# Performance work log

Hardware: AMD Instinct MI355X
Metric: run time of the kernel (lower is better)

## Reference

```python
import jax, jax.numpy as jnp
from jax import lax
import numpy as np

D_MODEL, D_STATE, D_CONV, EXPAND = 1024, 16, 4, 2
D_INNER = EXPAND * D_MODEL          # 2048
DT_RANK = D_MODEL // 16             # 64
B_SZ, L_SEQ = 2, 2048


def setup_inputs() -> dict:
    key = jax.random.key(0)
    ks = jax.random.split(key, 8)
    x = jax.random.normal(ks[0], (B_SZ, L_SEQ, D_MODEL), jnp.float32)
    inp = {
        "x": x,
        "ln_g": jnp.ones((D_MODEL,), jnp.float32),
        "ln_b": jnp.zeros((D_MODEL,), jnp.float32),
        # fan-in scaled weights for numerical sanity
        "W_in": jax.random.normal(ks[1], (2 * D_INNER, D_MODEL), jnp.float32) / np.sqrt(D_MODEL),
        "conv_w": jax.random.normal(ks[2], (D_INNER, D_CONV), jnp.float32) / np.sqrt(D_CONV),
        "conv_b": jnp.zeros((D_INNER,), jnp.float32),
        "W_xp": jax.random.normal(ks[3], (DT_RANK + 2 * D_STATE, D_INNER), jnp.float32) / np.sqrt(D_INNER),
        "W_dt": jax.random.normal(ks[4], (D_INNER, DT_RANK), jnp.float32) / np.sqrt(DT_RANK),
        "b_dt": jax.random.normal(ks[5], (D_INNER,), jnp.float32) * 0.1 - 4.0,  # softplus(dt) small, like mamba init
        # S4D-real init: A = -exp(A_log), A_log = log(1..d_state)
        "A_log": jnp.broadcast_to(jnp.log(jnp.arange(1, D_STATE + 1, dtype=jnp.float32)), (D_INNER, D_STATE)).copy(),
        "D": jnp.ones((D_INNER,), jnp.float32),
        "W_out": jax.random.normal(ks[6], (D_MODEL, D_INNER), jnp.float32) / np.sqrt(D_INNER),
    }
    return inp


def _selective_scan(u, dt, A, Bm, Cm, Dvec):
    # u, dt: (B, L, d_inner); Bm, Cm: (B, L, d_state); A: (d_inner, d_state)
    def step(h, inputs):
        u_t, dt_t, B_t, C_t = inputs                      # (B,di),(B,di),(B,n),(B,n)
        dA = jnp.exp(dt_t[:, :, None] * A[None])          # (B,di,n), in (0,1) since A<0
        dBu = (dt_t * u_t)[:, :, None] * B_t[:, None, :]  # (B,di,n)
        h = dA * h + dBu
        y = jnp.einsum('bdn,bn->bd', h, C_t)
        return h, y
    xs = (u.transpose(1, 0, 2), dt.transpose(1, 0, 2),
          Bm.transpose(1, 0, 2), Cm.transpose(1, 0, 2))
    h0 = jnp.zeros((u.shape[0], u.shape[2], A.shape[1]), u.dtype)
    _, ys = lax.scan(step, h0, xs)
    return ys.transpose(1, 0, 2) + u * Dvec               # (B, L, d_inner)


def reference(x, ln_g, ln_b, W_in, conv_w, conv_b, W_xp, W_dt, b_dt, A_log, D, W_out):
    d_inner, d_conv = conv_w.shape
    dt_rank = W_dt.shape[1]
    d_state = A_log.shape[1]
    # pre-LayerNorm
    mu = jnp.mean(x, axis=-1, keepdims=True)
    var = jnp.mean(jnp.square(x - mu), axis=-1, keepdims=True)
    xn = (x - mu) * lax.rsqrt(var + 1e-5) * ln_g + ln_b
    # input projection -> (B, L, 2*d_inner)
    xz = jnp.einsum('bld,ed->ble', xn, W_in)
    u, z = jnp.split(xz, 2, axis=-1)
    # causal depthwise conv over time
    u_c = lax.conv_general_dilated(
        u.transpose(0, 2, 1),                 # (B, d_inner, L)
        conv_w[:, None, :],                   # (d_inner, 1, d_conv)
        window_strides=(1,), padding=[(d_conv - 1, 0)],
        feature_group_count=d_inner)
    u_c = jax.nn.silu((u_c + conv_b[None, :, None]).transpose(0, 2, 1))  # (B, L, d_inner)
    # data-dependent dt, B, C
    x_dbl = jnp.einsum('bld,ed->ble', u_c, W_xp)
    dt, Bm, Cm = jnp.split(x_dbl, [dt_rank, dt_rank + d_state], axis=-1)
    dt = jax.nn.softplus(jnp.einsum('blr,dr->bld', dt, W_dt) + b_dt)
    A = -jnp.exp(A_log)
    y = _selective_scan(u_c, dt, A, Bm, Cm, D)
    y = y * jax.nn.silu(z)
    out = jnp.einsum('ble,de->bld', y, W_out)
    return x + out
```

## Files before the change

### kernel.cpp

```cpp
#include <hip/hip_runtime.h>

typedef __bf16 bf16x8 __attribute__((ext_vector_type(8)));
typedef float  f32x4  __attribute__((ext_vector_type(4)));

#define LOG2E 1.44269504088896f

__device__ __forceinline__ float bfl(unsigned short s) {
    return __uint_as_float(((unsigned int)s) << 16);
}
__device__ __forceinline__ unsigned short f2bf(float f) {
    unsigned int x = __float_as_uint(f);
    x += 0x7fffu + ((x >> 16) & 1u);
    return (unsigned short)(x >> 16);
}
__device__ __forceinline__ float fexp2(float x) { return __builtin_amdgcn_exp2f(x); }
__device__ __forceinline__ float fexp(float x)  { return __builtin_amdgcn_exp2f(x * LOG2E); }
__device__ __forceinline__ float frcp(float x)  { return __builtin_amdgcn_rcpf(x); }
__device__ __forceinline__ float silu_f(float x) {
    return x * frcp(1.f + fexp2(-x * LOG2E));
}
__device__ __forceinline__ void gl_lds(const unsigned short* g, unsigned short* l) {
    __builtin_amdgcn_global_load_lds(
        (__attribute__((address_space(1))) const void*)g,
        (__attribute__((address_space(3))) void*)l, 16, 0, 0);
}

#define BSZ   2
#define LSEQ  2048
#define DMODEL 1024
#define DI    2048
#define DS    16
#define NCH   64
#define CL    32

#define WI_N   4194304
#define WXP_N  196608
#define WDT_N  131072
#define WOUT_N 2097152
#define WSEG1  (WI_N)
#define WSEG2  (WI_N + WXP_N)
#define WSEG3  (WI_N + WXP_N + WDT_N)
#define WTOT   (WI_N + WXP_N + WDT_N + WOUT_N)

__global__ __launch_bounds__(256) void cvt_weights(
    const float* __restrict__ w0, const float* __restrict__ w1,
    const float* __restrict__ w2, const float* __restrict__ w3,
    unsigned short* __restrict__ dst)
{
    const size_t e0 = ((size_t)blockIdx.x * 256 + threadIdx.x) * 8;
    if (e0 >= WTOT) return;
    const float* src;
    size_t off;
    if      (e0 < WSEG1) { src = w0; off = e0; }
    else if (e0 < WSEG2) { src = w1; off = e0 - WSEG1; }
    else if (e0 < WSEG3) { src = w2; off = e0 - WSEG2; }
    else                 { src = w3; off = e0 - WSEG3; }
    float4 a = *(const float4*)(src + off);
    float4 b = *(const float4*)(src + off + 4);
    ushort4 lo, hi;
    lo.x = f2bf(a.x); lo.y = f2bf(a.y); lo.z = f2bf(a.z); lo.w = f2bf(a.w);
    hi.x = f2bf(b.x); hi.y = f2bf(b.y); hi.z = f2bf(b.z); hi.w = f2bf(b.w);
    *(ushort4*)(dst + e0) = lo;
    *(ushort4*)(dst + e0 + 4) = hi;
}

__global__ __launch_bounds__(256) void ln_kernel(
    const float* __restrict__ x,
    const float* __restrict__ g,
    const float* __restrict__ b,
    unsigned short* __restrict__ xn)
{
    const int row = blockIdx.x;
    const int tid = threadIdx.x;
    const int lane = tid & 63, wv = tid >> 6;
    const float* xp = x + (size_t)row * DMODEL;

    float4 v = ((const float4*)xp)[tid];
    float s = v.x + v.y + v.z + v.w;
    float q = v.x*v.x + v.y*v.y + v.z*v.z + v.w*v.w;
    #pragma unroll
    for (int o = 32; o > 0; o >>= 1) {
        s += __shfl_down(s, o);
        q += __shfl_down(q, o);
    }
    __shared__ float ss[4], sq[4];
    if (lane == 0) { ss[wv] = s; sq[wv] = q; }
    __syncthreads();
    s = ss[0] + ss[1] + ss[2] + ss[3];
    q = sq[0] + sq[1] + sq[2] + sq[3];
    const float mu  = s * (1.f / DMODEL);
    const float var = q * (1.f / DMODEL) - mu * mu;
    const float rs  = rsqrtf(var + 1e-5f);

    float4 gv = ((const float4*)g)[tid];
    float4 bv = ((const float4*)b)[tid];
    ushort4 o;
    o.x = f2bf((v.x - mu) * rs * gv.x + bv.x);
    o.y = f2bf((v.y - mu) * rs * gv.y + bv.y);
    o.z = f2bf((v.z - mu) * rs * gv.z + bv.z);
    o.w = f2bf((v.w - mu) * rs * gv.w + bv.w);
    ((ushort4*)(xn + (size_t)row * DMODEL))[tid] = o;
}

template<int EPI, int LOGM>
__global__ __launch_bounds__(512, 2) void gemm_pipe(
    const unsigned short* __restrict__ A,
    const unsigned short* __restrict__ Bw,
    void* __restrict__ Cout,
    const void* __restrict__ aux0,
    int K, int ldc)
{
    __shared__ unsigned short As[2][256 * 64];
    __shared__ unsigned short Bs[2][128 * 64];
    const int tid  = threadIdx.x;
    const int lane = tid & 63;
    const int wid  = tid >> 6;
    const int wm   = (wid >> 2) * 128;
    const int wn   = (wid & 3) * 32;

    const int nwg = gridDim.x;
    const int id  = blockIdx.x;
    const int swz = (id & 7) * (nwg >> 3) + (id >> 3);
    const int bx  = swz & ((1 << LOGM) - 1);
    const int by  = swz >> LOGM;
    const size_t am0 = (size_t)bx * 256;
    const size_t bn0 = (size_t)by * 128;

    const int srow  = lane >> 3;
    const int sslot = (lane & 7) ^ srow;
    const unsigned short* gA = A  + (am0 + wid * 32 + srow) * (size_t)K + sslot * 8;
    const unsigned short* gB = Bw + (bn0 + wid * 16 + srow) * (size_t)K + sslot * 8;
    unsigned short* lA0 = &As[0][(wid * 32) * 64];
    unsigned short* lB0 = &Bs[0][(wid * 16) * 64];
    unsigned short* lA1 = &As[1][(wid * 32) * 64];
    unsigned short* lB1 = &Bs[1][(wid * 16) * 64];

    const int NT = K >> 6;
    #pragma unroll
    for (int j = 0; j < 4; ++j) gl_lds(gA + (size_t)(8 * j) * K,       lA0 + j * 512);
    #pragma unroll
    for (int j = 0; j < 2; ++j) gl_lds(gB + (size_t)(8 * j) * K,       lB0 + j * 512);
    #pragma unroll
    for (int j = 0; j < 4; ++j) gl_lds(gA + (size_t)(8 * j) * K + 64,  lA1 + j * 512);
    #pragma unroll
    for (int j = 0; j < 2; ++j) gl_lds(gB + (size_t)(8 * j) * K + 64,  lB1 + j * 512);

    f32x4 acc[8][2];
    f32x4 z4 = {0.f, 0.f, 0.f, 0.f};
    #pragma unroll
    for (int i = 0; i < 8; ++i) { acc[i][0] = z4; acc[i][1] = z4; }

    const int lr  = lane & 15;
    const int lq  = lane >> 4;
    const int key = lr & 7;

    for (int t = 0; t < NT; ++t) {
        const int cur = t & 1;
        if (t < NT - 1) asm volatile("s_waitcnt vmcnt(6)" ::: "memory");
        else            asm volatile("s_waitcnt vmcnt(0)" ::: "memory");
        __builtin_amdgcn_s_barrier();
        __builtin_amdgcn_sched_barrier(0);

        bf16x8 af[8][2], bfv[2][2];
        #pragma unroll
        for (int fm = 0; fm < 8; ++fm)
            #pragma unroll
            for (int ks = 0; ks < 2; ++ks)
                af[fm][ks] = *(const bf16x8*)
                    &As[cur][(wm + fm * 16 + lr) * 64 + ((ks * 4 + lq) ^ key) * 8];
        #pragma unroll
        for (int fn = 0; fn < 2; ++fn)
            #pragma unroll
            for (int ks = 0; ks < 2; ++ks)
                bfv[fn][ks] = *(const bf16x8*)
                    &Bs[cur][(wn + fn * 16 + lr) * 64 + ((ks * 4 + lq) ^ key) * 8];
        asm volatile("s_waitcnt lgkmcnt(0)" ::: "memory");
        __builtin_amdgcn_sched_barrier(0);
        __builtin_amdgcn_s_barrier();

        if (t + 2 < NT) {
            const size_t ko = (size_t)(t + 2) * 64;
            unsigned short* dA = (cur ? lA1 : lA0);
            unsigned short* dB = (cur ? lB1 : lB0);
            #pragma unroll
            for (int j = 0; j < 4; ++j) gl_lds(gA + (size_t)(8 * j) * K + ko, dA + j * 512);
            #pragma unroll
            for (int j = 0; j < 2; ++j) gl_lds(gB + (size_t)(8 * j) * K + ko, dB + j * 512);
        }

        __builtin_amdgcn_s_setprio(1);
        #pragma unroll
        for (int fm = 0; fm < 8; ++fm)
            #pragma unroll
            for (int fn = 0; fn < 2; ++fn) {
                acc[fm][fn] = __builtin_amdgcn_mfma_f32_16x16x32_bf16(
                    af[fm][0], bfv[fn][0], acc[fm][fn], 0, 0, 0);
                acc[fm][fn] = __builtin_amdgcn_mfma_f32_16x16x32_bf16(
                    af[fm][1], bfv[fn][1], acc[fm][fn], 0, 0, 0);
            }
        __builtin_amdgcn_s_setprio(0);
    }

    const int er = lq * 4;
    const int ec = lr;
    #pragma unroll
    for (int fm = 0; fm < 8; ++fm) {
        #pragma unroll
        for (int fn = 0; fn < 2; ++fn) {
            const size_t col = bn0 + wn + fn * 16 + ec;
            #pragma unroll
            for (int r = 0; r < 4; ++r) {
                const size_t row = am0 + wm + fm * 16 + er + r;
                float v = acc[fm][fn][r];
                if constexpr (EPI == 0) {
                    ((unsigned short*)Cout)[row * ldc + col] = f2bf(v);
                } else {
                    float t2 = v + ((const float*)aux0)[row * ldc + col];
                    ((float*)Cout)[row * ldc + col] = t2;
                }
            }
        }
    }
}

template<int BM, int BN, int EPI, int LOG_NBXM>
__global__ __launch_bounds__(256) void gemm_lds(
    const unsigned short* __restrict__ A,
    const unsigned short* __restrict__ Bw,
    void* __restrict__ Cout,
    const void* __restrict__ aux0,
    int K, int ldc)
{
    constexpr int FM = BM / 32;
    constexpr int FN = BN / 32;
    __shared__ unsigned short As[BM * 64];
    __shared__ unsigned short Bs[BN * 64];
    const int tid  = threadIdx.x;
    const int lane = tid & 63;
    const int wv   = tid >> 6;
    const int wm   = (wv >> 1) * (BM / 2);
    const int wn   = (wv & 1)  * (BN / 2);

    const int nwg = gridDim.x;
    const int id  = blockIdx.x;
    const int swz = (id & 7) * (nwg >> 3) + (id >> 3);
    const int bx  = swz & ((1 << LOG_NBXM) - 1);
    const int by  = swz >> LOG_NBXM;

    f32x4 acc[FM][FN];
    f32x4 z4 = {0.f, 0.f, 0.f, 0.f};
    #pragma unroll
    for (int i = 0; i < FM; ++i)
        #pragma unroll
        for (int j = 0; j < FN; ++j) acc[i][j] = z4;

    const size_t am0 = (size_t)bx * BM;
    const size_t bn0 = (size_t)by * BN;
    const int srow  = lane >> 3;
    const int scol  = (lane & 7) * 8;

    for (int k0 = 0; k0 < K; k0 += 64) {
        __syncthreads();
        #pragma unroll
        for (int i = 0; i < BM / 32; ++i) {
            const int rb = (wv * (BM / 32) + i) * 8;
            gl_lds(&A[(am0 + rb + srow) * (size_t)K + k0 + scol], &As[rb * 64]);
        }
        #pragma unroll
        for (int i = 0; i < BN / 32; ++i) {
            const int rb = (wv * (BN / 32) + i) * 8;
            gl_lds(&Bw[(bn0 + rb + srow) * (size_t)K + k0 + scol], &Bs[rb * 64]);
        }
        __syncthreads();
        const int lr = lane & 15, lk = (lane >> 4) * 8;
        #pragma unroll
        for (int ks = 0; ks < 2; ++ks) {
            bf16x8 af[FM], bfv[FN];
            #pragma unroll
            for (int fm = 0; fm < FM; ++fm)
                af[fm] = *(const bf16x8*)&As[(wm + fm * 16 + lr) * 64 + ks * 32 + lk];
            #pragma unroll
            for (int fn = 0; fn < FN; ++fn)
                bfv[fn] = *(const bf16x8*)&Bs[(wn + fn * 16 + lr) * 64 + ks * 32 + lk];
            #pragma unroll
            for (int fm = 0; fm < FM; ++fm)
                #pragma unroll
                for (int fn = 0; fn < FN; ++fn)
                    acc[fm][fn] = __builtin_amdgcn_mfma_f32_16x16x32_bf16(
                        af[fm], bfv[fn], acc[fm][fn], 0, 0, 0);
        }
    }

    const int er = (lane >> 4) * 4;
    const int ec = lane & 15;
    #pragma unroll
    for (int fm = 0; fm < FM; ++fm) {
        #pragma unroll
        for (int fn = 0; fn < FN; ++fn) {
            const size_t col = bn0 + wn + fn * 16 + ec;
            #pragma unroll
            for (int r = 0; r < 4; ++r) {
                const size_t row = am0 + wm + fm * 16 + er + r;
                float v = acc[fm][fn][r];
                if constexpr (EPI == 0) {
                    ((unsigned short*)Cout)[row * ldc + col] = f2bf(v);
                } else if constexpr (EPI == 2) {
                    float t = v + ((const float*)aux0)[col];
                    float e = fexp2(t * LOG2E);
                    float sp = 0.69314718056f * __builtin_amdgcn_logf(1.f + e);
                    if (t > 20.f) sp = t;
                    ((unsigned short*)Cout)[row * ldc + col] = f2bf(sp);
                } else {
                    float t = v + ((const float*)aux0)[row * ldc + col];
                    ((float*)Cout)[row * ldc + col] = t;
                }
            }
        }
    }
}

__global__ __launch_bounds__(256) void gemm4_splitk(
    const unsigned short* __restrict__ A,
    const unsigned short* __restrict__ Bw,
    float* __restrict__ Cpart)
{
    constexpr int LDP = 72;
    __shared__ unsigned short As[64 * LDP];
    __shared__ unsigned short Bs[96 * LDP];
    const int tid  = threadIdx.x;
    const int lane = tid & 63;
    const int wv   = tid >> 6;
    const int wm   = (wv >> 1) * 32;
    const int wn   = (wv & 1)  * 48;

    f32x4 acc[2][3];
    f32x4 z4 = {0.f, 0.f, 0.f, 0.f};
    #pragma unroll
    for (int i = 0; i < 2; ++i)
        #pragma unroll
        for (int j = 0; j < 3; ++j) acc[i][j] = z4;

    const size_t am0 = (size_t)blockIdx.x * 64;
    const int kz = blockIdx.y;
    const int kbeg = kz * 256;
    const int r0 = tid >> 3;
    const int c0 = (tid & 7) * 8;

    for (int k0 = kbeg; k0 < kbeg + 256; k0 += 64) {
        __syncthreads();
        #pragma unroll
        for (int p = 0; p < 2; ++p) {
            int r = r0 + p * 32;
            *(uint4*)&As[r * LDP + c0] = *(const uint4*)&A[(am0 + r) * (size_t)2048 + k0 + c0];
        }
        #pragma unroll
        for (int p = 0; p < 3; ++p) {
            int r = r0 + p * 32;
            *(uint4*)&Bs[r * LDP + c0] = *(const uint4*)&Bw[(size_t)r * 2048 + k0 + c0];
        }
        __syncthreads();
        const int lr = lane & 15, lk = (lane >> 4) * 8;
        #pragma unroll
        for (int ks = 0; ks < 2; ++ks) {
            bf16x8 af[2], bfv[3];
            #pragma unroll
            for (int fm = 0; fm < 2; ++fm)
                af[fm] = *(const bf16x8*)&As[(wm + fm * 16 + lr) * LDP + ks * 32 + lk];
            #pragma unroll
            for (int fn = 0; fn < 3; ++fn)
                bfv[fn] = *(const bf16x8*)&Bs[(wn + fn * 16 + lr) * LDP + ks * 32 + lk];
            #pragma unroll
            for (int fm = 0; fm < 2; ++fm)
                #pragma unroll
                for (int fn = 0; fn < 3; ++fn)
                    acc[fm][fn] = __builtin_amdgcn_mfma_f32_16x16x32_bf16(
                        af[fm], bfv[fn], acc[fm][fn], 0, 0, 0);
        }
    }

    const int er = (lane >> 4) * 4;
    const int ec = lane & 15;
    float* out = Cpart + (size_t)kz * 4096 * 96;
    #pragma unroll
    for (int fm = 0; fm < 2; ++fm) {
        #pragma unroll
        for (int fn = 0; fn < 3; ++fn) {
            const int col = wn + fn * 16 + ec;
            #pragma unroll
            for (int r = 0; r < 4; ++r) {
                const size_t row = am0 + wm + fm * 16 + er + r;
                out[row * 96 + col] = acc[fm][fn][r];
            }
        }
    }
}

__global__ __launch_bounds__(256) void reduce_xdbl(
    const float* __restrict__ Cpart,
    float* __restrict__ x_dbl,
    unsigned short* __restrict__ dtlow)
{
    const int e = blockIdx.x * 256 + threadIdx.x;
    float s = 0.f;
    #pragma unroll
    for (int kz = 0; kz < 8; ++kz) s += Cpart[(size_t)kz * 393216 + e];
    x_dbl[e] = s;
    const int row = e / 96, col = e - row * 96;
    if (col < 64) dtlow[row * 64 + col] = f2bf(s);
}

__global__ __launch_bounds__(256) void conv_silu(
    const unsigned short* __restrict__ xz,
    const float* __restrict__ convw,
    const float* __restrict__ convb,
    unsigned short* __restrict__ u_c)
{
    const size_t i = (size_t)blockIdx.x * 256 + threadIdx.x;
    if (i >= (size_t)BSZ * LSEQ * DI) return;
    const int d = (int)(i & (DI - 1));
    const size_t bl = i >> 11;
    const int l = (int)(bl & (LSEQ - 1));
    const int b = (int)(bl >> 11);

    float4 wv = *(const float4*)&convw[d * 4];
    float acc = convb[d];
    const size_t rowbase = (size_t)(b * LSEQ) * (2 * DI) + d;
    if (l >= 3) acc += bfl(xz[rowbase + (size_t)(l - 3) * (2 * DI)]) * wv.x;
    if (l >= 2) acc += bfl(xz[rowbase + (size_t)(l - 2) * (2 * DI)]) * wv.y;
    if (l >= 1) acc += bfl(xz[rowbase + (size_t)(l - 1) * (2 * DI)]) * wv.z;
    acc += bfl(xz[rowbase + (size_t)l * (2 * DI)]) * wv.w;
    u_c[i] = f2bf(silu_f(acc));
}

__device__ __forceinline__ bool load_A(const float* __restrict__ A_log, int d, float* An2) {
    bool fast = true;
    #pragma unroll
    for (int i = 0; i < 4; ++i) {
        float4 a = *(const float4*)&A_log[(size_t)d * DS + i * 4];
        float e0 = fexp(a.x), e1 = fexp(a.y), e2 = fexp(a.z), e3 = fexp(a.w);
        fast = fast && fabsf(e0 - (4*i+1)) < 1e-3f * (4*i+1)
                    && fabsf(e1 - (4*i+2)) < 1e-3f * (4*i+2)
                    && fabsf(e2 - (4*i+3)) < 1e-3f * (4*i+3)
                    && fabsf(e3 - (4*i+4)) < 1e-3f * (4*i+4);
        An2[4*i+0] = -e0 * LOG2E; An2[4*i+1] = -e1 * LOG2E;
        An2[4*i+2] = -e2 * LOG2E; An2[4*i+3] = -e3 * LOG2E;
    }
    return fast;
}

__global__ __launch_bounds__(256) void scan1(
    const unsigned short* __restrict__ dt,
    const unsigned short* __restrict__ u_c,
    const float* __restrict__ x_dbl,
    const float* __restrict__ A_log,
    float* __restrict__ chunk_h,
    float* __restrict__ Ssum)
{
    const int d = blockIdx.x * 256 + threadIdx.x;
    const int b = blockIdx.y, c = blockIdx.z;
    const int tid = threadIdx.x;

    __shared__ float sB[CL][DS];
    if (tid < 128) {
        int s = tid >> 2, j = (tid & 3) * 4;
        *(float4*)&sB[s][j] =
            *(const float4*)&x_dbl[(size_t)(b * LSEQ + c * CL + s) * 96 + 64 + j];
    }

    float An2[DS];
    const bool fast = load_A(A_log, d, An2);
    __syncthreads();

    float h[DS];
    #pragma unroll
    for (int n = 0; n < DS; ++n) h[n] = 0.f;
    float S = 0.f;
    const size_t base = (size_t)(b * LSEQ + c * CL) * DI + d;
    if (fast) {
        for (int s = 0; s < CL; ++s) {
            float dtt = bfl(dt[base + (size_t)s * DI]);
            float ut  = bfl(u_c[base + (size_t)s * DI]);
            S += dtt;
            float dtu = dtt * ut;
            float e1 = fexp2(-dtt * LOG2E);
            float p = 1.f;
            #pragma unroll
            for (int n = 0; n < DS; ++n) {
                p *= e1;
                h[n] = p * h[n] + dtu * sB[s][n];
            }
        }
    } else {
        for (int s = 0; s < CL; ++s) {
            float dtt = bfl(dt[base + (size_t)s * DI]);
            float ut  = bfl(u_c[base + (size_t)s * DI]);
            S += dtt;
            float dtu = dtt * ut;
            #pragma unroll
            for (int n = 0; n < DS; ++n) {
                float dA = fexp2(dtt * An2[n]);
                h[n] = dA * h[n] + dtu * sB[s][n];
            }
        }
    }
    const size_t co = ((size_t)((b * NCH + c) * DI) + d) * DS;
    #pragma unroll
    for (int n = 0; n < DS; ++n) chunk_h[co + n] = h[n];
    Ssum[(size_t)(b * NCH + c) * DI + d] = S;
}

__global__ __launch_bounds__(256) void scan2(
    float* __restrict__ chunk_h,
    const float* __restrict__ Ssum,
    const float* __restrict__ A_log)
{
    const int gid = blockIdx.x * 256 + threadIdx.x;
    const int b = gid >> 15;
    const int rem = gid & 32767;
    const int d = rem >> 4;
    const int n = rem & 15;
    const float A2 = -fexp(A_log[(size_t)d * DS + n]) * LOG2E;
    float H = 0.f;
    for (int c = 0; c < NCH; ++c) {
        const size_t idx = ((size_t)((b * NCH + c) * DI) + d) * DS + n;
        float hl = chunk_h[idx];
        float S  = Ssum[(size_t)(b * NCH + c) * DI + d];
        chunk_h[idx] = H;
        H = fexp2(A2 * S) * H + hl;
    }
}

__global__ __launch_bounds__(256) void scan3(
    const unsigned short* __restrict__ dt,
    const unsigned short* __restrict__ u_c,
    const float* __restrict__ x_dbl,
    const float* __restrict__ A_log,
    const float* __restrict__ Hstart,
    const float* __restrict__ Dvec,
    const unsigned short* __restrict__ xz,
    unsigned short* __restrict__ yb)
{
    const int d = blockIdx.x * 256 + threadIdx.x;
    const int b = blockIdx.y, c = blockIdx.z;
    const int tid = threadIdx.x;

    __shared__ float sBC[CL][32];
    {
        int s = tid >> 3, j = (tid & 7) * 4;
        *(float4*)&sBC[s][j] =
            *(const float4*)&x_dbl[(size_t)(b * LSEQ + c * CL + s) * 96 + 64 + j];
    }

    float An2[DS];
    const bool fast = load_A(A_log, d, An2);
    const float Dd = Dvec[d];
    float h[DS];
    const size_t co = ((size_t)((b * NCH + c) * DI) + d) * DS;
    #pragma unroll
    for (int n = 0; n < DS; ++n) h[n] = Hstart[co + n];
    __syncthreads();

    const size_t base  = (size_t)(b * LSEQ + c * CL) * DI + d;
    const size_t zbase = (size_t)(b * LSEQ + c * CL) * (2 * DI) + DI + d;
    if (fast) {
        for (int s = 0; s < CL; ++s) {
            float dtt = bfl(dt[base + (size_t)s * DI]);
            float ut  = bfl(u_c[base + (size_t)s * DI]);
            float dtu = dtt * ut;
            float e1 = fexp2(-dtt * LOG2E);
            float p = 1.f;
            float a0 = 0.f, a1 = 0.f;
            #pragma unroll
            for (int n = 0; n < DS; ++n) {
                p *= e1;
                h[n] = p * h[n] + dtu * sBC[s][n];
                if (n & 1) a1 += h[n] * sBC[s][16 + n];
                else       a0 += h[n] * sBC[s][16 + n];
            }
            float y = a0 + a1 + Dd * ut;
            float z = bfl(xz[zbase + (size_t)s * (2 * DI)]);
            yb[base + (size_t)s * DI] = f2bf(y * silu_f(z));
        }
    } else {
        for (int s = 0; s < CL; ++s) {
            float dtt = bfl(dt[base + (size_t)s * DI]);
            float ut  = bfl(u_c[base + (size_t)s * DI]);
            float dtu = dtt * ut;
            float a0 = 0.f, a1 = 0.f;
            #pragma unroll
            for (int n = 0; n < DS; ++n) {
                float dA = fexp2(dtt * An2[n]);
                h[n] = dA * h[n] + dtu * sBC[s][n];
                if (n & 1) a1 += h[n] * sBC[s][16 + n];
                else       a0 += h[n] * sBC[s][16 + n];
            }
            float y = a0 + a1 + Dd * ut;
            float z = bfl(xz[zbase + (size_t)s * (2 * DI)]);
            yb[base + (size_t)s * DI] = f2bf(y * silu_f(z));
        }
    }
}

extern "C" void kernel_launch(void* const* d_in, const int* in_sizes, int n_in,
                              void* d_out, int out_size, void* d_ws, size_t ws_size,
                              hipStream_t stream) {
    const float* x      = (const float*)d_in[0];
    const float* ln_g   = (const float*)d_in[1];
    const float* ln_b   = (const float*)d_in[2];
    const float* W_in   = (const float*)d_in[3];
    const float* conv_w = (const float*)d_in[4];
    const float* conv_b = (const float*)d_in[5];
    const float* W_xp   = (const float*)d_in[6];
    const float* W_dt   = (const float*)d_in[7];
    const float* b_dt   = (const float*)d_in[8];
    const float* A_log  = (const float*)d_in[9];
    const float* Dv     = (const float*)d_in[10];
    const float* W_out  = (const float*)d_in[11];
    float* out = (float*)d_out;

    char* w = (char*)d_ws;
    unsigned short* xn     = (unsigned short*)(w + 0);
    unsigned short* xz     = (unsigned short*)(w + 8388608);
    unsigned short* u_c    = (unsigned short*)(w + 41943040);
    float*          x_dbl  = (float*)         (w + 58720256);
    unsigned short* dtlow  = (unsigned short*)(w + 60293120);
    unsigned short* dtb    = (unsigned short*)(w + 60817408);
    float*          chunkh = (float*)         (w + 77594624);
    float*          Ssum   = (float*)         (w + 94371840);
    unsigned short* yb     = (unsigned short*)(w + 95420416);
    unsigned short* wbf    = (unsigned short*)(w + 112197632);
    float*          Cpart  = (float*)         (w + 125435904);
    unsigned short* Wi_bf   = wbf;
    unsigned short* Wxp_bf  = wbf + WSEG1;
    unsigned short* Wdt_bf  = wbf + WSEG2;
    unsigned short* Wout_bf = wbf + WSEG3;
    (void)in_sizes; (void)n_in; (void)out_size; (void)ws_size;

    const int MROWS = BSZ * LSEQ;

    cvt_weights<<<(WTOT / 8 + 255) / 256, 256, 0, stream>>>(
        W_in, W_xp, W_dt, W_out, wbf);
    ln_kernel<<<MROWS, 256, 0, stream>>>(x, ln_g, ln_b, xn);
    gemm_pipe<0, 4><<<512, 512, 0, stream>>>(
        xn, Wi_bf, xz, nullptr, DMODEL, 2 * DI);
    conv_silu<<<(MROWS * DI) / 256, 256, 0, stream>>>(xz, conv_w, conv_b, u_c);
    gemm4_splitk<<<dim3(64, 8), 256, 0, stream>>>(u_c, Wxp_bf, Cpart);
    reduce_xdbl<<<(MROWS * 96) / 256, 256, 0, stream>>>(Cpart, x_dbl, dtlow);
    gemm_lds<128, 64, 2, 5><<<1024, 256, 0, stream>>>(
        dtlow, Wdt_bf, dtb, b_dt, 64, DI);
    scan1<<<dim3(DI / 256, BSZ, NCH), 256, 0, stream>>>(
        dtb, u_c, x_dbl, A_log, chunkh, Ssum);
    scan2<<<(BSZ * DI * DS) / 256, 256, 0, stream>>>(chunkh, Ssum, A_log);
    scan3<<<dim3(DI / 256, BSZ, NCH), 256, 0, stream>>>(
        dtb, u_c, x_dbl, A_log, chunkh, Dv, xz, yb);
    gemm_lds<128, 64, 3, 5><<<512, 256, 0, stream>>>(
        yb, Wout_bf, out, x, DI, DMODEL);
}
```

Before: 206.1 us.

## Enlarge input-projection GEMM tile to 256x256 with interleaved LDS reads and MFMA

The in-projection GEMM moves from a 256x128 to a 256x256 block tile, so each wave computes 128x64 outputs and the grid halves to 256 workgroups. The A-fragment LDS reads are split into four quarters and interleaved with the MFMA groups, so LDS latency is hidden behind compute and fewer fragment registers are live at once. The goal is more operand reuse per LDS byte and less global traffic. In exchange it uses 128KB of LDS per block (likely one block per CU), doubles the accumulator registers, and the 256-block grid only roughly matches the CU count, which can hurt load balance.

```diff
diff --git a/kernel.cpp b/kernel.cpp
--- a/kernel.cpp
+++ b/kernel.cpp
@@ -103,7 +103,7 @@
 }
 
 template<int EPI, int LOGM>
-__global__ __launch_bounds__(512, 2) void gemm_pipe(
+__global__ __launch_bounds__(512, 2) void gemm_pipe256(
     const unsigned short* __restrict__ A,
     const unsigned short* __restrict__ Bw,
     void* __restrict__ Cout,
@@ -111,12 +111,12 @@
     int K, int ldc)
 {
     __shared__ unsigned short As[2][256 * 64];
-    __shared__ unsigned short Bs[2][128 * 64];
+    __shared__ unsigned short Bs[2][256 * 64];
     const int tid  = threadIdx.x;
     const int lane = tid & 63;
     const int wid  = tid >> 6;
     const int wm   = (wid >> 2) * 128;
-    const int wn   = (wid & 3) * 32;
+    const int wn   = (wid & 3) * 64;
 
     const int nwg = gridDim.x;
     const int id  = blockIdx.x;
@@ -124,89 +124,112 @@
     const int bx  = swz & ((1 << LOGM) - 1);
     const int by  = swz >> LOGM;
     const size_t am0 = (size_t)bx * 256;
-    const size_t bn0 = (size_t)by * 128;
+    const size_t bn0 = (size_t)by * 256;
 
     const int srow  = lane >> 3;
     const int sslot = (lane & 7) ^ srow;
-    const unsigned short* gA = A  + (am0 + wid * 32 + srow) * (size_t)K + sslot * 8;
-    const unsigned short* gB = Bw + (bn0 + wid * 16 + srow) * (size_t)K + sslot * 8;
-    unsigned short* lA0 = &As[0][(wid * 32) * 64];
-    unsigned short* lB0 = &Bs[0][(wid * 16) * 64];
-    unsigned short* lA1 = &As[1][(wid * 32) * 64];
-    unsigned short* lB1 = &Bs[1][(wid * 16) * 64];
+    const unsigned short* gA = A  + (am0 + wid * 8 + srow) * (size_t)K + sslot * 8;
+    const unsigned short* gB = Bw + (bn0 + wid * 8 + srow) * (size_t)K + sslot * 8;
 
     const int NT = K >> 6;
-    #pragma unroll
-    for (int j = 0; j < 4; ++j) gl_lds(gA + (size_t)(8 * j) * K,       lA0 + j * 512);
-    #pragma unroll
-    for (int j = 0; j < 2; ++j) gl_lds(gB + (size_t)(8 * j) * K,       lB0 + j * 512);
-    #pragma unroll
-    for (int j = 0; j < 4; ++j) gl_lds(gA + (size_t)(8 * j) * K + 64,  lA1 + j * 512);
-    #pragma unroll
-    for (int j = 0; j < 2; ++j) gl_lds(gB + (size_t)(8 * j) * K + 64,  lB1 + j * 512);
-
-    f32x4 acc[8][2];
+
+#define STAGE256(buf, ko)                                                      \
+    {   _Pragma("unroll")                                                      \
+        for (int j = 0; j < 4; ++j)                                            \
+            gl_lds(gA + (size_t)(j * 64) * K + (ko), &As[buf][(j * 64 + wid * 8) * 64]); \
+        _Pragma("unroll")                                                      \
+        for (int j = 0; j < 4; ++j)                                            \
+            gl_lds(gB + (size_t)(j * 64) * K + (ko), &Bs[buf][(j * 64 + wid * 8) * 64]); }
+
+    STAGE256(0, 0)
+    STAGE256(1, 64)
+
+    f32x4 acc[8][4];
     f32x4 z4 = {0.f, 0.f, 0.f, 0.f};
     #pragma unroll
-    for (int i = 0; i < 8; ++i) { acc[i][0] = z4; acc[i][1] = z4; }
+    for (int i = 0; i < 8; ++i)
+        #pragma unroll
+        for (int j = 0; j < 4; ++j) acc[i][j] = z4;
 
     const int lr  = lane & 15;
     const int lq  = lane >> 4;
     const int key = lr & 7;
 
+#define RD_A(dst, q)                                                           \
+    _Pragma("unroll")                                                          \
+    for (int i = 0; i < 2; ++i)                                                \
+        _Pragma("unroll")                                                      \
+        for (int ks = 0; ks < 2; ++ks)                                         \
+            dst[i][ks] = *(const bf16x8*)&As[cur][(wm + ((q) * 2 + i) * 16 + lr) * 64 \
+                                                  + (((ks * 4 + lq) ^ key) * 8)];
+
+#define MFMA_Q(src, q)                                                         \
+    _Pragma("unroll")                                                          \
+    for (int i = 0; i < 2; ++i)                                                \
+        _Pragma("unroll")                                                      \
+        for (int fn = 0; fn < 4; ++fn) {                                       \
+            acc[(q) * 2 + i][fn] = __builtin_amdgcn_mfma_f32_16x16x32_bf16(    \
+                src[i][0], bfv[fn][0], acc[(q) * 2 + i][fn], 0, 0, 0);         \
+            acc[(q) * 2 + i][fn] = __builtin_amdgcn_mfma_f32_16x16x32_bf16(    \
+                src[i][1], bfv[fn][1], acc[(q) * 2 + i][fn], 0, 0, 0);         }
+
     for (int t = 0; t < NT; ++t) {
         const int cur = t & 1;
-        if (t < NT - 1) asm volatile("s_waitcnt vmcnt(6)" ::: "memory");
+        if (t < NT - 1) asm volatile("s_waitcnt vmcnt(8)" ::: "memory");
         else            asm volatile("s_waitcnt vmcnt(0)" ::: "memory");
         __builtin_amdgcn_s_barrier();
         __builtin_amdgcn_sched_barrier(0);
 
-        bf16x8 af[8][2], bfv[2][2];
-        #pragma unroll
-        for (int fm = 0; fm < 8; ++fm)
+        bf16x8 bfv[4][2], fA[2][2], fB[2][2];
+        #pragma unroll
+        for (int fn = 0; fn < 4; ++fn)
             #pragma unroll
             for (int ks = 0; ks < 2; ++ks)
-                af[fm][ks] = *(const bf16x8*)
-                    &As[cur][(wm + fm * 16 + lr) * 64 + ((ks * 4 + lq) ^ key) * 8];
-        #pragma unroll
-        for (int fn = 0; fn < 2; ++fn)
-            #pragma unroll
-            for (int ks = 0; ks < 2; ++ks)
-                bfv[fn][ks] = *(const bf16x8*)
-                    &Bs[cur][(wn + fn * 16 + lr) * 64 + ((ks * 4 + lq) ^ key) * 8];
+                bfv[fn][ks] = *(const bf16x8*)&Bs[cur][(wn + fn * 16 + lr) * 64
+                                                        + (((ks * 4 + lq) ^ key) * 8)];
+        RD_A(fA, 0)
         asm volatile("s_waitcnt lgkmcnt(0)" ::: "memory");
         __builtin_amdgcn_sched_barrier(0);
+
+        RD_A(fB, 1)
+        __builtin_amdgcn_s_setprio(1);
+        MFMA_Q(fA, 0)
+        __builtin_amdgcn_s_setprio(0);
+        asm volatile("s_waitcnt lgkmcnt(0)" ::: "memory");
+        __builtin_amdgcn_sched_barrier(0);
+
+        RD_A(fA, 2)
+        __builtin_amdgcn_s_setprio(1);
+        MFMA_Q(fB, 1)
+        __builtin_amdgcn_s_setprio(0);
+        asm volatile("s_waitcnt lgkmcnt(0)" ::: "memory");
+        __builtin_amdgcn_sched_barrier(0);
+
+        RD_A(fB, 3)
+        __builtin_amdgcn_s_setprio(1);
+        MFMA_Q(fA, 2)
+        __builtin_amdgcn_s_setprio(0);
+        asm volatile("s_waitcnt lgkmcnt(0)" ::: "memory");
+        __builtin_amdgcn_sched_barrier(0);
+
         __builtin_amdgcn_s_barrier();
-
         if (t + 2 < NT) {
-            const size_t ko = (size_t)(t + 2) * 64;
-            unsigned short* dA = (cur ? lA1 : lA0);
-            unsigned short* dB = (cur ? lB1 : lB0);
-            #pragma unroll
-            for (int j = 0; j < 4; ++j) gl_lds(gA + (size_t)(8 * j) * K + ko, dA + j * 512);
-            #pragma unroll
-            for (int j = 0; j < 2; ++j) gl_lds(gB + (size_t)(8 * j) * K + ko, dB + j * 512);
-        }
-
+            STAGE256(cur, (size_t)(t + 2) * 64)
+        }
         __builtin_amdgcn_s_setprio(1);
-        #pragma unroll
-        for (int fm = 0; fm < 8; ++fm)
-            #pragma unroll
-            for (int fn = 0; fn < 2; ++fn) {
-                acc[fm][fn] = __builtin_amdgcn_mfma_f32_16x16x32_bf16(
-                    af[fm][0], bfv[fn][0], acc[fm][fn], 0, 0, 0);
-                acc[fm][fn] = __builtin_amdgcn_mfma_f32_16x16x32_bf16(
-                    af[fm][1], bfv[fn][1], acc[fm][fn], 0, 0, 0);
-            }
+        MFMA_Q(fB, 3)
         __builtin_amdgcn_s_setprio(0);
     }
+#undef RD_A
+#undef MFMA_Q
+#undef STAGE256
 
     const int er = lq * 4;
     const int ec = lr;
     #pragma unroll
     for (int fm = 0; fm < 8; ++fm) {
         #pragma unroll
-        for (int fn = 0; fn < 2; ++fn) {
+        for (int fn = 0; fn < 4; ++fn) {
             const size_t col = bn0 + wn + fn * 16 + ec;
             #pragma unroll
             for (int r = 0; r < 4; ++r) {
@@ -641,7 +664,7 @@
     cvt_weights<<<(WTOT / 8 + 255) / 256, 256, 0, stream>>>(
         W_in, W_xp, W_dt, W_out, wbf);
     ln_kernel<<<MROWS, 256, 0, stream>>>(x, ln_g, ln_b, xn);
-    gemm_pipe<0, 4><<<512, 512, 0, stream>>>(
+    gemm_pipe256<0, 4><<<256, 512, 0, stream>>>(
         xn, Wi_bf, xz, nullptr, DMODEL, 2 * DI);
     conv_silu<<<(MROWS * DI) / 256, 256, 0, stream>>>(xz, conv_w, conv_b, u_c);
     gemm4_splitk<<<dim3(64, 8), 256, 0, stream>>>(u_c, Wxp_bf, Cpart);
```

New measurement: 195.3 us. -5.2%, faster.
